# Kernel optimization log

Measured on AMD Instinct MI355X. Metric: run time of the kernel, lower is better.

## Reference

```python
import jax, jax.numpy as jnp
import numpy as np

N = 100000
MUL = 16


def _build_cg():
    # Real-basis Clebsch-Gordan (Wigner-3j-style) coefficients, shape (2l1+1, 2l2+1, 2lo+1),
    # each normalized to unit Frobenius norm per output component (e3nn component normalization).
    eps = np.zeros((3, 3, 3), np.float32)
    for a, b, c in [(0, 1, 2), (1, 2, 0), (2, 0, 1)]:
        eps[a, b, c] = 1.0
        eps[a, c, b] = -1.0
    s2 = np.float32(1.0 / np.sqrt(2.0))
    q = np.zeros((5, 3, 3), np.float32)  # l=2 real harmonics: xy, yz, 3z^2-r^2, xz, x^2-y^2
    q[0, 0, 1] = q[0, 1, 0] = s2
    q[1, 1, 2] = q[1, 2, 1] = s2
    q[2] = np.diag([-1.0, -1.0, 2.0]).astype(np.float32) / np.sqrt(6.0)
    q[3, 0, 2] = q[3, 2, 0] = s2
    q[4] = np.diag([1.0, -1.0, 0.0]).astype(np.float32) * s2
    cg000 = jnp.ones((1, 1, 1), jnp.float32)                                   # 0e x 0e -> 0e
    cg011 = jnp.asarray(np.eye(3, dtype=np.float32)[None])                      # 0e x 1o -> 1o
    cg110 = jnp.asarray((np.eye(3, dtype=np.float32) / np.sqrt(3.0))[:, :, None])  # 1o x 1o -> 0e
    cg111 = jnp.asarray(eps * s2)                                               # 1o x 1o -> 1e
    cg112 = jnp.asarray(np.transpose(q, (1, 2, 0)))                             # 1o x 1o -> 2e
    return cg000, cg011, cg110, cg111, cg112


def _path(x1, x2, cg, w, alpha):
    # 'uvw' tensor-product path: out[z,w,m] = alpha * sum_{u,v,i,j} x1[z,u,i] x2[z,v,j] cg[i,j,m] w[u,v,w]
    # Contraction order chosen to keep the largest intermediate at [z,u,w,j].
    t = jnp.einsum('zvj,uvw->zuwj', x2, w)
    s = jnp.einsum('zui,zuwj->zwij', x1, t)
    return alpha * jnp.einsum('zwij,ijm->zwm', s, cg)


def _tensor_square(x, w0, w1, w2, w3, w4):
    n = x.shape[0]
    x0 = x[:, :MUL].reshape(n, MUL, 1)       # 16x0e
    x1 = x[:, MUL:].reshape(n, MUL, 3)       # 16x1o
    cg000, cg011, cg110, cg111, cg112 = _build_cg()
    a2 = 1.0 / np.sqrt(MUL * MUL * 2.0)      # 0e output receives 2 paths
    a1 = 1.0 / np.sqrt(MUL * MUL * 1.0)
    o_0e = _path(x0, x0, cg000, w0, a2) + _path(x1, x1, cg110, w2, a2)
    o_1o = _path(x0, x1, cg011, w1, a1)
    o_1e = _path(x1, x1, cg111, w3, a1)
    o_2e = _path(x1, x1, cg112, w4, a1)
    return jnp.concatenate([o.reshape(n, -1) for o in (o_0e, o_1o, o_1e, o_2e)], axis=1)


def setup_inputs() -> dict:
    key = jax.random.key(0)
    kx, k0, k1, k2, k3, k4 = jax.random.split(key, 6)
    return {
        'x': jax.random.normal(kx, (N, MUL * 1 + MUL * 3), jnp.float32),
        'w0': jax.random.normal(k0, (MUL, MUL, MUL), jnp.float32),
        'w1': jax.random.normal(k1, (MUL, MUL, MUL), jnp.float32),
        'w2': jax.random.normal(k2, (MUL, MUL, MUL), jnp.float32),
        'w3': jax.random.normal(k3, (MUL, MUL, MUL), jnp.float32),
        'w4': jax.random.normal(k4, (MUL, MUL, MUL), jnp.float32),
    }


def reference(x, w0, w1, w2, w3, w4):
    return _tensor_square(x, w0, w1, w2, w3, w4)
```

## Files before the change

kernel.cpp:

```cpp
#include <hip/hip_runtime.h>
#include <hip/hip_bf16.h>

typedef __attribute__((ext_vector_type(8))) short short8;
typedef __attribute__((ext_vector_type(4))) float float4v;
typedef __attribute__((ext_vector_type(2))) float float2v;
typedef __attribute__((ext_vector_type(4))) unsigned uint4v;

#define S_A 0.04419417382415922f
#define S_B 0.025515518153991442f
#define S_C 0.0625f
#define R_BA 0.5773502691896258f

static __device__ __forceinline__ unsigned pkbf(float a, float b) {
    unsigned r;
    asm("v_cvt_pk_bf16_f32 %0, %1, %2" : "=v"(r) : "v"(a), "v"(b));
    return r;
}

__global__ void wprep_kernel(const float* __restrict__ w0, const float* __restrict__ w1,
                             const float* __restrict__ w2, const float* __restrict__ w3,
                             const float* __restrict__ w4, unsigned short* __restrict__ wout)
{
    int e = blockIdx.x * 256 + threadIdx.x;
    if (e >= 64 * 512) return;
    int f = e >> 9;
    int r = e & 511;
    int lane = r >> 3, j = r & 7;

    const float* wp;
    float scl;
    int c;
    if (f < 24)      { c = f / 3;        int i = f % 3;
                       wp  = (i == 0) ? w0 : (i == 1) ? w2 : w4;
                       scl = (i == 1) ? S_B : S_A; }
    else if (f < 48) { int fp = f - 24;  c = fp / 3; int i = fp % 3;
                       wp  = (i == 0) ? w1 : (i == 1) ? w3 : w4;
                       scl = (i == 0) ? S_C : S_A; }
    else             { int fp = f - 48;  c = fp / 2; int i = fp % 2;
                       wp  = (i == 0) ? w3 : w4;
                       scl = S_A; }

    int k = c * 32 + ((lane >> 4) << 3) + j;
    int wcol = lane & 15;
    unsigned u = __builtin_bit_cast(unsigned, scl * wp[k * 16 + wcol]);
    u += 0x7fffu + ((u >> 16) & 1u);
    wout[(f * 64 + lane) * 8 + j] = (unsigned short)(u >> 16);
}

template<int G>
static __device__ __forceinline__ void run_group(
    const float* __restrict__ xr, int l, const short8* __restrict__ wbase,
    float* __restrict__ out, long long z0)
{
    const int g  = l >> 4;
    const int v0 = (g & 1) * 8;
    const int uo = g >> 1;

    float2v Xv[4], Yv[4], Zv[4];
    float2v A0v[4];
    {
        float b[24];
        #pragma unroll
        for (int q = 0; q < 6; q++)
            *(float4v*)&b[q * 4] = *(const float4v*)(xr + 16 + v0 * 3 + q * 4);
        #pragma unroll
        for (int t = 0; t < 4; t++) {
            Xv[t] = (float2v){b[6 * t + 0], b[6 * t + 3]};
            Yv[t] = (float2v){b[6 * t + 1], b[6 * t + 4]};
            Zv[t] = (float2v){b[6 * t + 2], b[6 * t + 5]};
        }
        if constexpr (G == 0) {
            float a[8];
            #pragma unroll
            for (int q = 0; q < 2; q++)
                *(float4v*)&a[q * 4] = *(const float4v*)(xr + v0 + q * 4);
            #pragma unroll
            for (int t = 0; t < 4; t++) A0v[t] = (float2v){a[2 * t], a[2 * t + 1]};
        }
    }

    constexpr int NS = (G == 1) ? 5 : 4;
    constexpr int NP = (G == 2) ? 2 : 3;
    constexpr int GBASE = (G == 0) ? 0 : (G == 1) ? 24 : 48;

    float4v acc[NS];
    #pragma unroll
    for (int s = 0; s < NS; s++) acc[s] = (float4v){0.f, 0.f, 0.f, 0.f};

    #pragma unroll
    for (int c = 0; c < 8; c++) {
        short8 wf[NP];
        #pragma unroll
        for (int i = 0; i < NP; i++) wf[i] = wbase[(GBASE + c * NP + i) * 64 + l];

        const int u = c * 2 + uo;
        float u0 = 0.f, ux = 0.f, uy, uz;
        if constexpr (G != 2) u0 = xr[u];
        if constexpr (G != 1) ux = xr[16 + u * 3 + 0];
        uy = xr[16 + u * 3 + 1];
        uz = xr[16 + u * 3 + 2];

        unsigned fri[NS][4];
        #pragma unroll
        for (int t = 0; t < 4; t++) {
            const float2v X = Xv[t], Y = Yv[t], Z = Zv[t];
            if constexpr (G == 0) {
                float2v b0  = u0 * A0v[t];
                float2v p00 = ux * X, p11 = uy * Y, p22 = uz * Z;
                float2v t01 = p00 + p11;
                float2v b1  = t01 + p22;
                float2v b10 = 2.0f * p22 - t01;
                float2v b12 = p00 - p11;
                fri[0][t] = pkbf(b0.x, b0.y);
                fri[1][t] = pkbf(b1.x, b1.y);
                fri[2][t] = pkbf(b10.x, b10.y);
                fri[3][t] = pkbf(b12.x, b12.y);
            }
            if constexpr (G == 1) {
                float2v b2 = u0 * X, b3 = u0 * Y, b4 = u0 * Z;
                float2v p12 = uy * Z;
                float2v b5 = p12 - uz * Y;
                float2v b9 = p12 + uz * Y;
                fri[0][t] = pkbf(b2.x, b2.y);
                fri[1][t] = pkbf(b3.x, b3.y);
                fri[2][t] = pkbf(b4.x, b4.y);
                fri[3][t] = pkbf(b5.x, b5.y);
                fri[4][t] = pkbf(b9.x, b9.y);
            }
            if constexpr (G == 2) {
                float2v p01 = ux * Y;
                float2v b7  = p01 - uy * X;
                float2v b8  = p01 + uy * X;
                float2v p02 = ux * Z;
                float2v b6  = uz * X - p02;
                float2v b11 = p02 + uz * X;
                fri[0][t] = pkbf(b6.x, b6.y);
                fri[1][t] = pkbf(b7.x, b7.y);
                fri[2][t] = pkbf(b8.x, b8.y);
                fri[3][t] = pkbf(b11.x, b11.y);
            }
        }

        #pragma unroll
        for (int s = 0; s < NS; s++) {
            short8 frm = __builtin_bit_cast(short8, *(uint4v*)fri[s]);
            int wi;
            if constexpr (G == 0) wi = (s == 0) ? 0 : (s == 1) ? 1 : 2;
            if constexpr (G == 1) wi = (s <= 2) ? 0 : (s == 3) ? 1 : 2;
            if constexpr (G == 2) wi = (s <= 1) ? 0 : 1;
            acc[s] = __builtin_amdgcn_mfma_f32_16x16x32_bf16(frm, wf[wi], acc[s], 0, 0, 0);
        }
    }

    const int w = l & 15;
    float* outp = out + (z0 + g * 4) * 192;
    #pragma unroll
    for (int reg = 0; reg < 4; reg++) {
        float* rowp = outp + reg * 192;
        if constexpr (G == 0) {
            rowp[w]               = acc[0][reg] + acc[1][reg];
            rowp[112 + w * 5 + 2] = R_BA * acc[2][reg];
            rowp[112 + w * 5 + 4] = acc[3][reg];
        }
        if constexpr (G == 1) {
            rowp[16 + w * 3 + 0]  = acc[0][reg];
            rowp[16 + w * 3 + 1]  = acc[1][reg];
            rowp[16 + w * 3 + 2]  = acc[2][reg];
            rowp[64 + w * 3 + 0]  = acc[3][reg];
            rowp[112 + w * 5 + 1] = acc[4][reg];
        }
        if constexpr (G == 2) {
            rowp[64 + w * 3 + 1]  = acc[0][reg];
            rowp[64 + w * 3 + 2]  = acc[1][reg];
            rowp[112 + w * 5 + 0] = acc[2][reg];
            rowp[112 + w * 5 + 3] = acc[3][reg];
        }
    }
}

__global__ __launch_bounds__(192, 4)
void tsq_kernel(const float* __restrict__ x,
                const unsigned short* __restrict__ wfrag,
                float* __restrict__ out,
                int nrows)
{
    __shared__ __attribute__((aligned(16))) float xlds[16 * 68];

    const int tid = threadIdx.x;
    const long long z0 = (long long)blockIdx.x * 16;

    {
        const float* xg = x + z0 * 64;
        {
            int f = tid * 4;
            int row = f >> 6, col = f & 63;
            float4v v = {0.f, 0.f, 0.f, 0.f};
            if (z0 + row < nrows) v = *(const float4v*)(xg + f);
            *(float4v*)&xlds[row * 68 + col] = v;
        }
        if (tid < 64) {
            int f = 768 + tid * 4;
            int row = f >> 6, col = f & 63;
            float4v v = {0.f, 0.f, 0.f, 0.f};
            if (z0 + row < nrows) v = *(const float4v*)(xg + f);
            *(float4v*)&xlds[row * 68 + col] = v;
        }
    }
    __syncthreads();
    if (z0 >= nrows) return;

    const int wave = tid >> 6;
    const int l = tid & 63;
    const float* xr = &xlds[(l & 15) * 68];
    const short8* wbase = (const short8*)wfrag;

    if      (wave == 0) run_group<0>(xr, l, wbase, out, z0);
    else if (wave == 1) run_group<1>(xr, l, wbase, out, z0);
    else                run_group<2>(xr, l, wbase, out, z0);
}

extern "C" void kernel_launch(void* const* d_in, const int* in_sizes, int n_in,
                              void* d_out, int out_size, void* d_ws, size_t ws_size,
                              hipStream_t stream) {
    const float* x  = (const float*)d_in[0];
    const float* w0 = (const float*)d_in[1];
    const float* w1 = (const float*)d_in[2];
    const float* w2 = (const float*)d_in[3];
    const float* w3 = (const float*)d_in[4];
    const float* w4 = (const float*)d_in[5];
    float* out = (float*)d_out;
    unsigned short* wfrag = (unsigned short*)d_ws;
    (void)ws_size; (void)n_in; (void)out_size;

    const int nrows = in_sizes[0] / 64;
    const int nblocks = (nrows + 15) / 16;

    wprep_kernel<<<dim3(128), dim3(256), 0, stream>>>(w0, w1, w2, w3, w4, wfrag);
    tsq_kernel<<<dim3(nblocks), dim3(192), 0, stream>>>(x, wfrag, out, nrows);
}
```

Measured before the change: 122.3 us.

## Load x rows directly into registers, dropping LDS staging and barrier

Each lane now loads its full 64-float input row from global memory into registers (16 float4 loads) instead of staging the 16-row tile through shared memory behind a __syncthreads. Per-u scalars are then taken from registers rather than LDS reads. The change also relaxes the launch bounds minimum-blocks hint, allowing more registers per thread. It removes LDS traffic and the barrier, but adds redundant global loads (16 lanes per row, three waves) and higher register pressure that may reduce occupancy.

```diff
diff --git a/kernel.cpp b/kernel.cpp
--- a/kernel.cpp
+++ b/kernel.cpp
@@ -49,34 +49,33 @@
 
 template<int G>
 static __device__ __forceinline__ void run_group(
-    const float* __restrict__ xr, int l, const short8* __restrict__ wbase,
+    const float* __restrict__ xrow, int l, const short8* __restrict__ wbase,
     float* __restrict__ out, long long z0)
 {
     const int g  = l >> 4;
     const int v0 = (g & 1) * 8;
     const int uo = g >> 1;
 
-    float2v Xv[4], Yv[4], Zv[4];
-    float2v A0v[4];
-    {
-        float b[24];
-        #pragma unroll
-        for (int q = 0; q < 6; q++)
-            *(float4v*)&b[q * 4] = *(const float4v*)(xr + 16 + v0 * 3 + q * 4);
-        #pragma unroll
-        for (int t = 0; t < 4; t++) {
-            Xv[t] = (float2v){b[6 * t + 0], b[6 * t + 3]};
-            Yv[t] = (float2v){b[6 * t + 1], b[6 * t + 4]};
-            Zv[t] = (float2v){b[6 * t + 2], b[6 * t + 5]};
-        }
-        if constexpr (G == 0) {
-            float a[8];
-            #pragma unroll
-            for (int q = 0; q < 2; q++)
-                *(float4v*)&a[q * 4] = *(const float4v*)(xr + v0 + q * 4);
-            #pragma unroll
-            for (int t = 0; t < 4; t++) A0v[t] = (float2v){a[2 * t], a[2 * t + 1]};
-        }
+    float4v q1[12];
+    #pragma unroll
+    for (int q = 0; q < 12; q++) q1[q] = *(const float4v*)(xrow + 16 + q * 4);
+    float4v q0[4];
+    if constexpr (G != 2) {
+        #pragma unroll
+        for (int q = 0; q < 4; q++) q0[q] = *(const float4v*)(xrow + q * 4);
+    }
+    auto R1 = [&](int i) { return q1[i >> 2][i & 3]; };
+    auto R0 = [&](int i) { return q0[i >> 2][i & 3]; };
+
+    float2v Xv[4], Yv[4], Zv[4], A0v[4];
+    #pragma unroll
+    for (int t = 0; t < 4; t++) {
+        const int ca = (v0 + 2 * t) * 3, cb = (v0 + 2 * t + 1) * 3;
+        Xv[t] = (float2v){R1(ca + 0), R1(cb + 0)};
+        Yv[t] = (float2v){R1(ca + 1), R1(cb + 1)};
+        Zv[t] = (float2v){R1(ca + 2), R1(cb + 2)};
+        if constexpr (G == 0)
+            A0v[t] = (float2v){R0(v0 + 2 * t), R0(v0 + 2 * t + 1)};
     }
 
     constexpr int NS = (G == 1) ? 5 : 4;
@@ -93,12 +92,12 @@
         #pragma unroll
         for (int i = 0; i < NP; i++) wf[i] = wbase[(GBASE + c * NP + i) * 64 + l];
 
-        const int u = c * 2 + uo;
+        const int uc = 2 * c + uo;
         float u0 = 0.f, ux = 0.f, uy, uz;
-        if constexpr (G != 2) u0 = xr[u];
-        if constexpr (G != 1) ux = xr[16 + u * 3 + 0];
-        uy = xr[16 + u * 3 + 1];
-        uz = xr[16 + u * 3 + 2];
+        if constexpr (G != 2) u0 = R0(uc);
+        if constexpr (G != 1) ux = R1(3 * uc + 0);
+        uy = R1(3 * uc + 1);
+        uz = R1(3 * uc + 2);
 
         unsigned fri[NS][4];
         #pragma unroll
@@ -178,45 +177,26 @@
     }
 }
 
-__global__ __launch_bounds__(192, 4)
+__global__ __launch_bounds__(192)
 void tsq_kernel(const float* __restrict__ x,
                 const unsigned short* __restrict__ wfrag,
                 float* __restrict__ out,
                 int nrows)
 {
-    __shared__ __attribute__((aligned(16))) float xlds[16 * 68];
-
     const int tid = threadIdx.x;
     const long long z0 = (long long)blockIdx.x * 16;
-
-    {
-        const float* xg = x + z0 * 64;
-        {
-            int f = tid * 4;
-            int row = f >> 6, col = f & 63;
-            float4v v = {0.f, 0.f, 0.f, 0.f};
-            if (z0 + row < nrows) v = *(const float4v*)(xg + f);
-            *(float4v*)&xlds[row * 68 + col] = v;
-        }
-        if (tid < 64) {
-            int f = 768 + tid * 4;
-            int row = f >> 6, col = f & 63;
-            float4v v = {0.f, 0.f, 0.f, 0.f};
-            if (z0 + row < nrows) v = *(const float4v*)(xg + f);
-            *(float4v*)&xlds[row * 68 + col] = v;
-        }
-    }
-    __syncthreads();
     if (z0 >= nrows) return;
 
     const int wave = tid >> 6;
     const int l = tid & 63;
-    const float* xr = &xlds[(l & 15) * 68];
+    long long row = z0 + (l & 15);
+    if (row >= nrows) row = nrows - 1;
+    const float* xrow = x + row * 64;
     const short8* wbase = (const short8*)wfrag;
 
-    if      (wave == 0) run_group<0>(xr, l, wbase, out, z0);
-    else if (wave == 1) run_group<1>(xr, l, wbase, out, z0);
-    else                run_group<2>(xr, l, wbase, out, z0);
+    if      (wave == 0) run_group<0>(xrow, l, wbase, out, z0);
+    else if (wave == 1) run_group<1>(xrow, l, wbase, out, z0);
+    else                run_group<2>(xrow, l, wbase, out, z0);
 }
 
 extern "C" void kernel_launch(void* const* d_in, const int* in_sizes, int n_in,
```

New measurement: 224.5 us. 83.6% more time.
